# Optimization experiments

Measured on AMD Instinct MI355X. Metric: run time of the kernel, lower is better.

The kernel has to match this reference:

```python
import jax, jax.numpy as jnp
import numpy as np

NUM_LABELS = 64
BATCH = 1024
SEQ_LEN = 512


def setup_inputs() -> dict:
    key = jax.random.key(0)
    k1, k2, k3, k4 = jax.random.split(key, 4)
    emissions = jax.random.normal(k1, (BATCH, SEQ_LEN, NUM_LABELS), dtype=jnp.float32)
    mask = jnp.ones((BATCH, SEQ_LEN), dtype=jnp.int32)
    # params: uniform(-0.1, 0.1) as in nn.init.uniform_
    transitions = jax.random.uniform(k2, (NUM_LABELS, NUM_LABELS), minval=-0.1, maxval=0.1, dtype=jnp.float32)
    start_transitions = jax.random.uniform(k3, (NUM_LABELS,), minval=-0.1, maxval=0.1, dtype=jnp.float32)
    end_transitions = jax.random.uniform(k4, (NUM_LABELS,), minval=-0.1, maxval=0.1, dtype=jnp.float32)
    return {
        "emissions": emissions,
        "mask": mask,
        "transitions": transitions,
        "start_transitions": start_transitions,
        "end_transitions": end_transitions,
    }


def reference(emissions, mask, transitions, start_transitions, end_transitions):
    """CRF forward algorithm (log partition) -> [batch]."""
    # initial alpha: start + emissions at t=0  -> [B, L]
    score0 = start_transitions + emissions[:, 0]

    # scan over time steps 1..S-1
    emit_rest = jnp.swapaxes(emissions[:, 1:], 0, 1)          # [S-1, B, L]
    mask_rest = jnp.swapaxes(mask[:, 1:], 0, 1)               # [S-1, B]

    def step(score, xs):
        emit_t, mask_t = xs                                   # [B, L], [B]
        # [B, L_prev, 1] + [L_prev, L_next] + [B, 1, L_next]
        next_score = jax.nn.logsumexp(
            score[:, :, None] + transitions[None] + emit_t[:, None, :], axis=1
        )                                                     # [B, L]
        score = jnp.where(mask_t[:, None].astype(bool), next_score, score)
        return score, None

    score, _ = jax.lax.scan(step, score0, (emit_rest, mask_rest))
    return jax.nn.logsumexp(score + end_transitions, axis=1)  # [B]
```

## Files before the change

### kernel.cpp

```cpp
#include <hip/hip_runtime.h>

#define NL 64
#define SQ 512
#define BATCH 1024
#define TMID 256

__device__ __forceinline__ float lane_bcast(float v, int lane) {
    return __uint_as_float(__builtin_amdgcn_readlane(__float_as_uint(v), lane));
}
__device__ __forceinline__ float lane0_bcast(float v) {
    return __uint_as_float(__builtin_amdgcn_readfirstlane(__float_as_uint(v)));
}

__global__ __launch_bounds__(64, 2) void crf_scan(
    const float* __restrict__ emissions,
    const int*   __restrict__ mask,
    const float* __restrict__ trans,
    const float* __restrict__ start_t,
    const float* __restrict__ end_t,
    float* __restrict__ ws_p,
    float* __restrict__ ws_c)
{
    const int  blk = blockIdx.x;
    const bool fwd = blk < BATCH;
    const int  b   = fwd ? blk : blk - BATCH;
    const int  j   = threadIdx.x;

    const float* em = emissions + (size_t)b * SQ * NL;
    const int*   mk = mask + (size_t)b * SQ;

    float et[NL];
    if (fwd) {
#pragma unroll
        for (int i = 0; i < NL; ++i) et[i] = __expf(trans[i * NL + j]);
    } else {
#pragma unroll
        for (int i = 0; i < NL; ++i) et[i] = __expf(trans[j * NL + i]);
    }

    auto matvec = [&](float y) {
        float a0 = 0.f, a1 = 0.f, a2 = 0.f, a3 = 0.f;
#pragma unroll
        for (int i = 0; i < NL; i += 4) {
            a0 = fmaf(lane_bcast(y, i + 0), et[i + 0], a0);
            a1 = fmaf(lane_bcast(y, i + 1), et[i + 1], a1);
            a2 = fmaf(lane_bcast(y, i + 2), et[i + 2], a2);
            a3 = fmaf(lane_bcast(y, i + 3), et[i + 3], a3);
        }
        return (a0 + a1) + (a2 + a3);
    };

    float p, logC;

    if (fwd) {
        const float s0 = start_t[j] + em[j];
        const float C  = lane0_bcast(s0);
        p = __expf(s0 - C);  logC = C;

        float r0 = em[1 * NL + j], r1 = em[2 * NL + j];
        float r2 = em[3 * NL + j], r3 = em[4 * NL + j];

        for (int g = 0; g < 63; ++g) {
            const int t = 1 + 4 * g;
            const float e0 = __expf(r0), e1 = __expf(r1);
            const float e2 = __expf(r2), e3 = __expf(r3);
            int t7 = t + 7; if (t7 > TMID - 1) t7 = TMID - 1;
            r0 = em[(t + 4) * NL + j]; r1 = em[(t + 5) * NL + j];
            r2 = em[(t + 6) * NL + j]; r3 = em[t7 * NL + j];
            const int m0 = mk[t], m1 = mk[t + 1], m2 = mk[t + 2], m3 = mk[t + 3];
            { const float pn = e0 * matvec(p); p = m0 ? pn : p; }
            { const float pn = e1 * matvec(p); p = m1 ? pn : p; }
            { const float pn = e2 * matvec(p); p = m2 ? pn : p; }
            { const float pn = e3 * matvec(p); p = m3 ? pn : p; }
            const float c0 = lane0_bcast(p);
            logC += __logf(c0);
            p *= __builtin_amdgcn_rcpf(c0);
        }
        const float e0 = __expf(r0), e1 = __expf(r1), e2 = __expf(r2);
        { const float pn = e0 * matvec(p); p = mk[253] ? pn : p; }
        { const float pn = e1 * matvec(p); p = mk[254] ? pn : p; }
        { const float pn = e2 * matvec(p); p = mk[255] ? pn : p; }
    } else {
        p = __expf(end_t[j]);  logC = 0.f;

        float r0 = em[511 * NL + j], r1 = em[510 * NL + j];
        float r2 = em[509 * NL + j], r3 = em[508 * NL + j];

        for (int g = 0; g < 64; ++g) {
            const int t = 511 - 4 * g;
            const float e0 = __expf(r0), e1 = __expf(r1);
            const float e2 = __expf(r2), e3 = __expf(r3);
            int t4 = t - 4, t5 = t - 5, t6 = t - 6, t7 = t - 7;
            if (t4 < TMID) t4 = TMID;  if (t5 < TMID) t5 = TMID;
            if (t6 < TMID) t6 = TMID;  if (t7 < TMID) t7 = TMID;
            r0 = em[t4 * NL + j]; r1 = em[t5 * NL + j];
            r2 = em[t6 * NL + j]; r3 = em[t7 * NL + j];
            const int m0 = mk[t], m1 = mk[t - 1], m2 = mk[t - 2], m3 = mk[t - 3];
            { const float pn = matvec(e0 * p); p = m0 ? pn : p; }
            { const float pn = matvec(e1 * p); p = m1 ? pn : p; }
            { const float pn = matvec(e2 * p); p = m2 ? pn : p; }
            { const float pn = matvec(e3 * p); p = m3 ? pn : p; }
            const float c0 = lane0_bcast(p);
            logC += __logf(c0);
            p *= __builtin_amdgcn_rcpf(c0);
        }
    }

    ws_p[(size_t)blk * NL + j] = p;
    if (j == 0) ws_c[blk] = logC;
}

__global__ __launch_bounds__(64) void crf_combine(
    const float* __restrict__ ws_p, const float* __restrict__ ws_c,
    float* __restrict__ out)
{
    const int b = blockIdx.x;
    const int j = threadIdx.x;
    float v = ws_p[(size_t)b * NL + j] * ws_p[(size_t)(b + BATCH) * NL + j];
#pragma unroll
    for (int off = 32; off; off >>= 1) v += __shfl_xor(v, off);
    if (j == 0) out[b] = ws_c[b] + ws_c[b + BATCH] + __logf(v);
}

extern "C" void kernel_launch(void* const* d_in, const int* in_sizes, int n_in,
                              void* d_out, int out_size, void* d_ws, size_t ws_size,
                              hipStream_t stream) {
    const float* emissions = (const float*)d_in[0];
    const int*   mask      = (const int*)d_in[1];
    const float* trans     = (const float*)d_in[2];
    const float* start_t   = (const float*)d_in[3];
    const float* end_t     = (const float*)d_in[4];
    float* out = (float*)d_out;

    float* ws_p = (float*)d_ws;
    float* ws_c = ws_p + 2 * BATCH * NL;

    crf_scan<<<2 * BATCH, NL, 0, stream>>>(emissions, mask, trans,
                                           start_t, end_t, ws_p, ws_c);
    crf_combine<<<BATCH, NL, 0, stream>>>(ws_p, ws_c, out);
}
```

Before: 284.0 us.

## Use packed fp16 dot2 matvec with per-step renormalization in CRF scan

Stores exp(transitions) as packed fp16 pairs and computes the matvec with v_dot2 instructions, broadcasting pairs of probabilities with one readlane each. This halves the readlane and FMA count on the serial recurrence. To keep values within fp16 range it renormalizes every step by lane 0 scaled by 1/4, and it tracks the log constant in base 2. The cost is a per-step readfirstlane, rcp and log on the critical path, plus reduced precision in the transition products.

```diff
diff --git a/kernel.cpp b/kernel.cpp
--- a/kernel.cpp
+++ b/kernel.cpp
@@ -5,11 +5,17 @@
 #define BATCH 1024
 #define TMID 256
 
-__device__ __forceinline__ float lane_bcast(float v, int lane) {
-    return __uint_as_float(__builtin_amdgcn_readlane(__float_as_uint(v), lane));
-}
+typedef __fp16 hf2 __attribute__((ext_vector_type(2)));
+
+#define EXP2F(x)  __builtin_amdgcn_exp2f(x)
+#define LOG2F(x)  __builtin_amdgcn_logf(x)
+
 __device__ __forceinline__ float lane0_bcast(float v) {
     return __uint_as_float(__builtin_amdgcn_readfirstlane(__float_as_uint(v)));
+}
+__device__ __forceinline__ hf2 bc2(int pki, int lane) {
+    int v = __builtin_amdgcn_readlane(pki, lane);
+    return __builtin_bit_cast(hf2, v);
 }
 
 __global__ __launch_bounds__(64, 2) void crf_scan(
@@ -25,89 +31,96 @@
     const bool fwd = blk < BATCH;
     const int  b   = fwd ? blk : blk - BATCH;
     const int  j   = threadIdx.x;
+    const float LOG2E = 1.44269504088896340736f;
 
     const float* em = emissions + (size_t)b * SQ * NL;
     const int*   mk = mask + (size_t)b * SQ;
 
-    float et[NL];
-    if (fwd) {
+    hf2 et2[NL / 2];
 #pragma unroll
-        for (int i = 0; i < NL; ++i) et[i] = __expf(trans[i * NL + j]);
-    } else {
-#pragma unroll
-        for (int i = 0; i < NL; ++i) et[i] = __expf(trans[j * NL + i]);
+    for (int k = 0; k < NL / 2; ++k) {
+        float e0, e1;
+        if (fwd) { e0 = __expf(trans[(2*k + 0) * NL + j]);
+                   e1 = __expf(trans[(2*k + 1) * NL + j]); }
+        else     { e0 = __expf(trans[j * NL + (2*k + 0)]);
+                   e1 = __expf(trans[j * NL + (2*k + 1)]); }
+        et2[k] = __builtin_amdgcn_cvt_pkrtz(e0, e1);
     }
 
-    auto matvec = [&](float y) {
+    auto matvec = [&](float xb) -> float {
+        int nb = __builtin_amdgcn_update_dpp(0, __float_as_int(xb),
+                                             0xB1, 0xF, 0xF, true);
+        hf2 pk = __builtin_amdgcn_cvt_pkrtz(xb, __int_as_float(nb));
+        int pki = __builtin_bit_cast(int, pk);
         float a0 = 0.f, a1 = 0.f, a2 = 0.f, a3 = 0.f;
 #pragma unroll
-        for (int i = 0; i < NL; i += 4) {
-            a0 = fmaf(lane_bcast(y, i + 0), et[i + 0], a0);
-            a1 = fmaf(lane_bcast(y, i + 1), et[i + 1], a1);
-            a2 = fmaf(lane_bcast(y, i + 2), et[i + 2], a2);
-            a3 = fmaf(lane_bcast(y, i + 3), et[i + 3], a3);
+        for (int k = 0; k < 32; k += 4) {
+            a0 = __builtin_amdgcn_fdot2(bc2(pki, 2*(k+0)), et2[k+0], a0, false);
+            a1 = __builtin_amdgcn_fdot2(bc2(pki, 2*(k+1)), et2[k+1], a1, false);
+            a2 = __builtin_amdgcn_fdot2(bc2(pki, 2*(k+2)), et2[k+2], a2, false);
+            a3 = __builtin_amdgcn_fdot2(bc2(pki, 2*(k+3)), et2[k+3], a3, false);
         }
         return (a0 + a1) + (a2 + a3);
     };
 
-    float p, logC;
+    float p, logC2;
 
     if (fwd) {
-        const float s0 = start_t[j] + em[j];
-        const float C  = lane0_bcast(s0);
-        p = __expf(s0 - C);  logC = C;
+        const float s0f = start_t[j] + em[j];
+        const float C   = lane0_bcast(s0f);
+        p = EXP2F((s0f - C) * LOG2E);  logC2 = C * LOG2E;
 
-        float r0 = em[1 * NL + j], r1 = em[2 * NL + j];
-        float r2 = em[3 * NL + j], r3 = em[4 * NL + j];
+        auto step = [&](float r, int m) {
+            const float ex   = EXP2F(r * LOG2E);
+            const float p0   = lane0_bcast(p);
+            const float sinv = 0.25f * __builtin_amdgcn_rcpf(p0);
+            const float mv   = matvec(p * sinv);
+            if (m) { p = ex * mv; logC2 += LOG2F(p0) + 2.0f; }
+        };
+
+        float r0 = em[1*NL + j], r1 = em[2*NL + j];
+        float r2 = em[3*NL + j], r3 = em[4*NL + j];
 
         for (int g = 0; g < 63; ++g) {
             const int t = 1 + 4 * g;
-            const float e0 = __expf(r0), e1 = __expf(r1);
-            const float e2 = __expf(r2), e3 = __expf(r3);
+            const float e0 = r0, e1 = r1, e2 = r2, e3 = r3;
             int t7 = t + 7; if (t7 > TMID - 1) t7 = TMID - 1;
-            r0 = em[(t + 4) * NL + j]; r1 = em[(t + 5) * NL + j];
-            r2 = em[(t + 6) * NL + j]; r3 = em[t7 * NL + j];
-            const int m0 = mk[t], m1 = mk[t + 1], m2 = mk[t + 2], m3 = mk[t + 3];
-            { const float pn = e0 * matvec(p); p = m0 ? pn : p; }
-            { const float pn = e1 * matvec(p); p = m1 ? pn : p; }
-            { const float pn = e2 * matvec(p); p = m2 ? pn : p; }
-            { const float pn = e3 * matvec(p); p = m3 ? pn : p; }
-            const float c0 = lane0_bcast(p);
-            logC += __logf(c0);
-            p *= __builtin_amdgcn_rcpf(c0);
+            r0 = em[(t+4)*NL + j]; r1 = em[(t+5)*NL + j];
+            r2 = em[(t+6)*NL + j]; r3 = em[t7*NL + j];
+            const int m0 = mk[t], m1 = mk[t+1], m2 = mk[t+2], m3 = mk[t+3];
+            step(e0, m0); step(e1, m1); step(e2, m2); step(e3, m3);
         }
-        const float e0 = __expf(r0), e1 = __expf(r1), e2 = __expf(r2);
-        { const float pn = e0 * matvec(p); p = mk[253] ? pn : p; }
-        { const float pn = e1 * matvec(p); p = mk[254] ? pn : p; }
-        { const float pn = e2 * matvec(p); p = mk[255] ? pn : p; }
+        step(r0, mk[253]); step(r1, mk[254]); step(r2, mk[255]);
     } else {
-        p = __expf(end_t[j]);  logC = 0.f;
+        p = __expf(end_t[j]);  logC2 = 0.f;
 
-        float r0 = em[511 * NL + j], r1 = em[510 * NL + j];
-        float r2 = em[509 * NL + j], r3 = em[508 * NL + j];
+        auto step = [&](float r, int m) {
+            const float ex   = EXP2F(r * LOG2E);
+            const float sc   = ex * p;
+            const float s0   = lane0_bcast(sc);
+            const float sinv = 0.25f * __builtin_amdgcn_rcpf(s0);
+            const float mv   = matvec(sc * sinv);
+            if (m) { p = mv; logC2 += LOG2F(s0) + 2.0f; }
+        };
+
+        float r0 = em[511*NL + j], r1 = em[510*NL + j];
+        float r2 = em[509*NL + j], r3 = em[508*NL + j];
 
         for (int g = 0; g < 64; ++g) {
             const int t = 511 - 4 * g;
-            const float e0 = __expf(r0), e1 = __expf(r1);
-            const float e2 = __expf(r2), e3 = __expf(r3);
-            int t4 = t - 4, t5 = t - 5, t6 = t - 6, t7 = t - 7;
+            const float e0 = r0, e1 = r1, e2 = r2, e3 = r3;
+            int t4 = t-4, t5 = t-5, t6 = t-6, t7 = t-7;
             if (t4 < TMID) t4 = TMID;  if (t5 < TMID) t5 = TMID;
             if (t6 < TMID) t6 = TMID;  if (t7 < TMID) t7 = TMID;
-            r0 = em[t4 * NL + j]; r1 = em[t5 * NL + j];
-            r2 = em[t6 * NL + j]; r3 = em[t7 * NL + j];
-            const int m0 = mk[t], m1 = mk[t - 1], m2 = mk[t - 2], m3 = mk[t - 3];
-            { const float pn = matvec(e0 * p); p = m0 ? pn : p; }
-            { const float pn = matvec(e1 * p); p = m1 ? pn : p; }
-            { const float pn = matvec(e2 * p); p = m2 ? pn : p; }
-            { const float pn = matvec(e3 * p); p = m3 ? pn : p; }
-            const float c0 = lane0_bcast(p);
-            logC += __logf(c0);
-            p *= __builtin_amdgcn_rcpf(c0);
+            r0 = em[t4*NL + j]; r1 = em[t5*NL + j];
+            r2 = em[t6*NL + j]; r3 = em[t7*NL + j];
+            const int m0 = mk[t], m1 = mk[t-1], m2 = mk[t-2], m3 = mk[t-3];
+            step(e0, m0); step(e1, m1); step(e2, m2); step(e3, m3);
         }
     }
 
     ws_p[(size_t)blk * NL + j] = p;
-    if (j == 0) ws_c[blk] = logC;
+    if (j == 0) ws_c[blk] = logC2;
 }
 
 __global__ __launch_bounds__(64) void crf_combine(
@@ -119,7 +132,9 @@
     float v = ws_p[(size_t)b * NL + j] * ws_p[(size_t)(b + BATCH) * NL + j];
 #pragma unroll
     for (int off = 32; off; off >>= 1) v += __shfl_xor(v, off);
-    if (j == 0) out[b] = ws_c[b] + ws_c[b + BATCH] + __logf(v);
+    if (j == 0)
+        out[b] = 0.69314718055994530942f *
+                 (ws_c[b] + ws_c[b + BATCH] + LOG2F(v));
 }
 
 extern "C" void kernel_launch(void* const* d_in, const int* in_sizes, int n_in,
```

After: 249.4 us. 1.14x faster.
